# Optimization experiments

Hardware: AMD Instinct MI355X
Metric: run time of the kernel (lower is better)

Reference implementation:

```python
import jax, jax.numpy as jnp
import numpy as np
from jax import lax

# Static config (matches init_kwargs)
DIM = 256; DR = 4; GROUP = 2; NH = 4; KS = 3; NA = 1; NUM_CLASS = 80; MUL = 5.0
CR = DIM // DR            # reduced dim = 64
GC = CR // GROUP          # offset-group channels = 32
HC = CR // NH             # per-head dim = 16
SCALE = HC ** -0.5
B, H, W = 8, 64, 64


def setup_inputs() -> dict:
    key = jax.random.key(0)
    ks_ = jax.random.split(key, 8)
    x = jax.random.normal(ks_[0], (B, DIM, H, W), jnp.float32)
    # offset = absolute pixel coordinates of the base sampling grid
    offset = jax.random.uniform(ks_[1], (B, NA * 2 * KS * KS, H, W), jnp.float32) * (H - 1)
    return dict(
        x=x, offset=offset,
        ln1_g=jnp.ones((DIM,), jnp.float32), ln1_b=jnp.zeros((DIM,), jnp.float32),
        w_qkv=jax.random.normal(ks_[2], (3 * CR, DIM), jnp.float32) * 0.02,
        w_dw=jax.random.normal(ks_[3], (GC, 1, 3, 3), jnp.float32) * 0.1,
        ln2_g=jnp.ones((GC,), jnp.float32), ln2_b=jnp.zeros((GC,), jnp.float32),
        w_off=jax.random.normal(ks_[4], (NA * 2 * KS * KS, GC, 3, 3), jnp.float32) * 0.02,
        b_off=jnp.zeros((NA * 2 * KS * KS,), jnp.float32),
        rpb_table=jax.random.normal(ks_[5], (1, NH, 1, 1, KS * KS, HC), jnp.float32) * 0.02,
        w_proj=jax.random.normal(ks_[6], (DIM, CR), jnp.float32) * 0.02,
        b_proj=jnp.zeros((DIM,), jnp.float32),
        w_cls=jax.random.normal(ks_[7], (NUM_CLASS, DIM), jnp.float32) * 0.02,
        b_cls=jnp.zeros((NUM_CLASS,), jnp.float32),
    )


def _ln_chw(x, g, b, eps=1e-5):
    # LayerNorm over channel dim of NCHW tensor (LayerNormProxy)
    xt = jnp.moveaxis(x, 1, -1)
    m = xt.mean(-1, keepdims=True)
    v = ((xt - m) ** 2).mean(-1, keepdims=True)
    y = (xt - m) * lax.rsqrt(v + eps) * g + b
    return jnp.moveaxis(y, -1, 1)


def _conv(x, w, groups=1, pad=1):
    return lax.conv_general_dilated(x, w, (1, 1), [(pad, pad), (pad, pad)],
                                    feature_group_count=groups,
                                    dimension_numbers=('NCHW', 'OIHW', 'NCHW'))


def _grid_sample(img, grid):
    # img [N,C,H,W]; grid [N,Ho,Wo,2] with (x,y) in [-1,1]; bilinear, zeros pad, align_corners=True
    N, C, Hi, Wi = img.shape
    gx = (grid[..., 0] + 1.0) * 0.5 * (Wi - 1)
    gy = (grid[..., 1] + 1.0) * 0.5 * (Hi - 1)
    x0 = jnp.floor(gx); y0 = jnp.floor(gy)
    x1 = x0 + 1.0;      y1 = y0 + 1.0

    def gather(ix, iy):
        valid = (ix >= 0) & (ix <= Wi - 1) & (iy >= 0) & (iy <= Hi - 1)
        ixc = jnp.clip(ix, 0, Wi - 1).astype(jnp.int32)
        iyc = jnp.clip(iy, 0, Hi - 1).astype(jnp.int32)
        v = jax.vmap(lambda im, yy, xx: im[:, yy, xx])(img, iyc, ixc)  # [N,C,Ho,Wo]
        return v * valid[:, None].astype(img.dtype)

    wa = ((x1 - gx) * (y1 - gy))[:, None]
    wb = ((gx - x0) * (y1 - gy))[:, None]
    wc = ((x1 - gx) * (gy - y0))[:, None]
    wd = ((gx - x0) * (gy - y0))[:, None]
    return (gather(x0, y0) * wa + gather(x1, y0) * wb +
            gather(x0, y1) * wc + gather(x1, y1) * wd)


def _extract_feats(feat, off, Hh, Ww):
    # feat [Bg,GC,H,W]; off [Bg, NA*2*KS*KS, H, W] in pixel coords (row, col)
    Bg = feat.shape[0]
    o = off.reshape(Bg, NA, KS, KS, 2, Hh, Ww)
    o = o.transpose(0, 1, 2, 5, 3, 6, 4)                  # b na kh h kw w d
    o = o.reshape(Bg, NA * KS * Hh, KS * Ww, 2)
    gy = 2.0 * o[..., 0] / (Hh - 1) - 1.0                  # row coord
    gx = 2.0 * o[..., 1] / (Ww - 1) - 1.0                  # col coord
    grid = jnp.stack([gx, gy], -1)                         # flip(-1): (x, y)
    out = _grid_sample(feat, grid)                         # [Bg,GC,NA*KS*H,KS*W]
    out = out.reshape(Bg, GC, NA, KS, Hh, KS, Ww)
    out = out.transpose(0, 2, 3, 5, 1, 4, 6).reshape(Bg, NA * KS * KS, GC, Hh, Ww)
    return out


def reference(x, offset, ln1_g, ln1_b, w_qkv, w_dw, ln2_g, ln2_b, w_off, b_off,
              rpb_table, w_proj, b_proj, w_cls, b_cls):
    Bb, C, Hh, Ww = x.shape
    N = KS * KS

    x_ = _ln_chw(x, ln1_g, ln1_b)
    qkv = jnp.einsum('oc,bchw->bohw', w_qkv, x_)           # [B,3*CR,H,W]
    q, k, v = jnp.split(qkv, 3, axis=1)                    # each [B,CR,H,W]

    # --- offset prediction ---
    q_off = q.reshape(Bb * GROUP, GC, Hh, Ww)
    t = _conv(q_off, w_dw, groups=GC)                      # depthwise 3x3
    t = _ln_chw(t, ln2_g, ln2_b)
    t = jax.nn.gelu(t, approximate=False)
    pred_offset = _conv(t, w_off) + b_off[None, :, None, None]

    off = jnp.broadcast_to(offset[:, None], (Bb, GROUP, NA * 2 * N, Hh, Ww))
    off = off.reshape(Bb * GROUP, NA * 2 * N, Hh, Ww)
    off = jnp.tanh(pred_offset) * MUL + off

    # --- deformable gather of k/v ---
    k = _extract_feats(k.reshape(Bb * GROUP, GC, Hh, Ww), off, Hh, Ww)
    v = _extract_feats(v.reshape(Bb * GROUP, GC, Hh, Ww), off, Hh, Ww)

    def to_heads(t):
        # [(b g), na*n, gc, h, w] -> [b, nh, hw, na, n, hc]
        t = t.reshape(Bb, GROUP, NA, N, GC, Hh, Ww)
        t = t.transpose(0, 5, 6, 2, 3, 1, 4)               # b h w na n g gc
        t = t.reshape(Bb, Hh * Ww, NA, N, NH, HC)
        return t.transpose(0, 4, 1, 2, 3, 5)

    k = to_heads(k) + rpb_table                            # [B,NH,HW,NA,N,HC]
    v = to_heads(v)

    q = q.reshape(Bb, NH, HC, Hh * Ww).transpose(0, 1, 3, 2)  # [B,NH,HW,HC]
    q = jnp.broadcast_to((q * SCALE)[:, :, :, None, :], (Bb, NH, Hh * Ww, NA, HC))

    attn = jnp.einsum('bnpac,bnpakc->bnpak', q, k)         # [B,NH,HW,NA,N]
    attn = jax.nn.softmax(attn, axis=-1)
    out = jnp.einsum('bnpak,bnpakc->bnpac', attn, v)       # [B,NH,HW,NA,HC]

    out = out.transpose(0, 2, 3, 1, 4).reshape(Bb, Hh * Ww, NA, CR)
    out = out @ w_proj.T + b_proj                          # [B,HW,NA,C]
    out = out + x.transpose(0, 2, 3, 1).reshape(Bb, Hh * Ww, 1, C)

    cls = out @ w_cls.T + b_cls                            # [B,HW,NA,NUM_CLASS]
    cls = cls.reshape(Bb, Hh, Ww, NA, NUM_CLASS).transpose(0, 3, 4, 1, 2)
    return cls.reshape(Bb, NA * NUM_CLASS, Hh, Ww)
```

## Files before the change

kernel.cpp:

```cpp
#include <hip/hip_runtime.h>
#include <hip/hip_fp16.h>
#include <math.h>

#define BB   8
#define HW   4096
#define BHW  32768
#define DIM  256
#define CR   64
#define GC   32
#define NHD  4
#define HC   16
#define NTAP 9
#define NCLS 80

#define OFF_QP   0u
#define OFF_QT   2097152u
#define OFF_KT   4194304u
#define OFF_WBF  8388608u
#define OFF_AB   8437760u
#define OFF_T16  8650752u
#define OFF_OFFB 10485760u
#define OFF_WPT  13762560u
#define OFF_WCT  13778944u
#define OFF_WFT  13799424u

typedef short    bf16x8 __attribute__((ext_vector_type(8)));
typedef _Float16 f16x8  __attribute__((ext_vector_type(8)));
typedef float    f32x4  __attribute__((ext_vector_type(4)));

__device__ __forceinline__ unsigned short f2bf(float f) {
    unsigned u = __float_as_uint(f);
    unsigned r = u + 0x7FFFu + ((u >> 16) & 1u);
    return (unsigned short)(r >> 16);
}

__global__ __launch_bounds__(256) void k0_prep(
    const float* __restrict__ wqkv, const float* __restrict__ g1,
    const float* __restrict__ b1, const float* __restrict__ woff,
    const float* __restrict__ wproj, const float* __restrict__ wcls,
    float* __restrict__ ws)
{
    const int t = threadIdx.x;
    const int blk = blockIdx.x;
    if (blk < 192) {
        const int o = blk;
        unsigned short* wbf = (unsigned short*)(ws + OFF_WBF);
        wbf[o * 256 + t] = f2bf(wqkv[o * 256 + t] * g1[t]);
    } else if (blk < 448) {
        const int r = blk - 192;
        unsigned short* wpb = (unsigned short*)(ws + OFF_WPT);
        unsigned short* wcb = (unsigned short*)(ws + OFF_WCT);
        if (t < 64) wpb[r * 64 + t] = f2bf(wproj[r * 64 + t]);
        if (r < 80) wcb[r * 256 + t] = f2bf(wcls[r * 256 + t]);
    } else if (blk < 640) {
        const int o = blk - 448;
        __shared__ float sa[4], sb[4];
        float w = wqkv[o * 256 + t];
        float a = w * g1[t];
        float bb = w * b1[t];
        #pragma unroll
        for (int off = 1; off < 64; off <<= 1) {
            a  += __shfl_xor(a,  off, 64);
            bb += __shfl_xor(bb, off, 64);
        }
        const int wv = t >> 6;
        if ((t & 63) == 0) { sa[wv] = a; sb[wv] = bb; }
        __syncthreads();
        if (t == 0) {
            ws[OFF_AB + o]       = sa[0] + sa[1] + sa[2] + sa[3];
            ws[OFF_AB + 192 + o] = sb[0] + sb[1] + sb[2] + sb[3];
        }
    } else {
        int idx = (blk - 640) * 256 + t;
        if (idx < 2 * 9 * 64 * 8) {
            int j = idx & 7;
            int lane = (idx >> 3) & 63;
            int mw = idx >> 9;
            int m = mw / 9, wo = mw % 9;
            int o = m * 16 + (lane & 15);
            int ic = (lane >> 4) * 8 + j;
            float v = (o < 18) ? woff[(o * 32 + ic) * 9 + wo] : 0.f;
            ((__half*)(ws + OFF_WFT))[idx] = __float2half(v);
        }
    }
}

__global__ __launch_bounds__(512) void k1_mfma(
    const float* __restrict__ x, float* __restrict__ ws)
{
    __shared__ float tile[64 * 193];
    const int t = threadIdx.x;
    const int b = blockIdx.x & 7, row = blockIdx.x >> 3;
    const int wv = __builtin_amdgcn_readfirstlane(t >> 6);
    const int pt = wv & 3, oh = wv >> 2;
    const int lane = t & 63;
    const int quad = lane >> 4, pxl = lane & 15;
    const int colbase = row * 64 + pt * 16 + pxl;
    const unsigned short* wbf = (const unsigned short*)(ws + OFF_WBF);
    const float* AB = ws + OFF_AB;

    f32x4 acc[6];
    #pragma unroll
    for (int ot = 0; ot < 6; ++ot) acc[ot] = (f32x4){0.f, 0.f, 0.f, 0.f};
    float s = 0.f, ss = 0.f;
    const size_t xb0 = (size_t)b * DIM * HW + colbase;

    for (int ks = 0; ks < 8; ++ks) {
        const int cbase = ks * 32 + quad * 8;
        float xv[8];
        #pragma unroll
        for (int j = 0; j < 8; ++j) {
            xv[j] = x[xb0 + (size_t)(cbase + j) * HW];
            s += xv[j]; ss += xv[j] * xv[j];
        }
        union { bf16x8 v; unsigned short u[8]; } bfrag;
        #pragma unroll
        for (int j = 0; j < 8; ++j) bfrag.u[j] = f2bf(xv[j]);
        #pragma unroll
        for (int ot = 0; ot < 6; ++ot) {
            const int orow = (oh * 6 + ot) * 16 + pxl;
            union { float4 f; bf16x8 v; } afrag;
            afrag.f = *(const float4*)&wbf[orow * 256 + cbase];
            acc[ot] = __builtin_amdgcn_mfma_f32_16x16x32_bf16(afrag.v, bfrag.v, acc[ot], 0, 0, 0);
        }
    }

    s  += __shfl_xor(s, 16, 64);  s  += __shfl_xor(s, 32, 64);
    ss += __shfl_xor(ss, 16, 64); ss += __shfl_xor(ss, 32, 64);
    const float m = s * (1.f / 256.f);
    const float rsv = rsqrtf(ss * (1.f / 256.f) - m * m + 1e-5f);

    const int px = pt * 16 + pxl;
    #pragma unroll
    for (int ot = 0; ot < 6; ++ot) {
        #pragma unroll
        for (int r = 0; r < 4; ++r) {
            int o = (oh * 6 + ot) * 16 + quad * 4 + r;
            tile[px * 193 + o] = rsv * (acc[ot][r] - m * AB[o]) + AB[192 + o];
        }
    }
    __syncthreads();

    float*  qp  = ws + OFF_QP;
    __half* qth = (__half*)(ws + OFF_QT);
    __half* kvh = (__half*)(ws + OFF_KT);
    const int colrow = row * 64;
    #pragma unroll
    for (int it = 0; it < 8; ++it) {
        int idx = it * 512 + t;
        int o = idx >> 6, px2 = idx & 63;
        qp[(size_t)(b * 64 + o) * HW + colrow + px2] = tile[px2 * 193 + o];
    }
    #pragma unroll
    for (int it = 0; it < 8; ++it) {
        int idx = it * 512 + t;
        int px2 = idx >> 6, o = idx & 63;
        qth[(size_t)(b * HW + colrow + px2) * 64 + o] = __float2half(tile[px2 * 193 + o]);
    }
    #pragma unroll
    for (int it = 0; it < 4; ++it) {
        int idx = it * 512 + t;
        int px2 = idx >> 5, ch32 = idx & 31;
        int sB = ch32 >> 4, ch = ch32 & 15;
        kvh[(size_t)((2 * b) * HW + colrow + px2) * 64 + sB * 32 + ch]
            = __float2half(tile[px2 * 193 + 64 + ch32]);
    }
    #pragma unroll
    for (int it = 0; it < 4; ++it) {
        int idx = it * 512 + t;
        int px2 = idx >> 5, ch32 = idx & 31;
        int sB = ch32 >> 4, ch = ch32 & 15;
        kvh[(size_t)((2 * b + 1) * HW + colrow + px2) * 64 + sB * 32 + ch]
            = __float2half(tile[px2 * 193 + 96 + ch32]);
    }
    #pragma unroll
    for (int it = 0; it < 4; ++it) {
        int idx = it * 512 + t;
        int px2 = idx >> 5, ch32 = idx & 31;
        int sB = ch32 >> 4, ch = ch32 & 15;
        kvh[(size_t)((2 * b) * HW + colrow + px2) * 64 + sB * 32 + 16 + ch]
            = __float2half(tile[px2 * 193 + 128 + ch32]);
    }
    #pragma unroll
    for (int it = 0; it < 4; ++it) {
        int idx = it * 512 + t;
        int px2 = idx >> 5, ch32 = idx & 31;
        int sB = ch32 >> 4, ch = ch32 & 15;
        kvh[(size_t)((2 * b + 1) * HW + colrow + px2) * 64 + sB * 32 + 16 + ch]
            = __float2half(tile[px2 * 193 + 160 + ch32]);
    }
}

__global__ __launch_bounds__(256) void k2_off_feat(
    const float* __restrict__ wdw, const float* __restrict__ g2, const float* __restrict__ b2,
    float* __restrict__ ws)
{
    __shared__ float qtile[3][32][64];
    __shared__ float rsum[4][64], rsq[4][64], smv[64], srv[64];
    const int t = threadIdx.x;
    const int b = blockIdx.x & 7;
    const int rest = blockIdx.x >> 3;
    const int g = rest & 1;
    const int row = rest >> 1;
    const int bg = b * 2 + g;
    const int p = t & 63;
    const int cq = __builtin_amdgcn_readfirstlane(t >> 6);
    const float* qp = ws + OFF_QP;

    #pragma unroll
    for (int it = 0; it < 6; ++it) {
        int idx = it * 256 + t;
        int rc = idx >> 4;
        int seg = (idx & 15) << 2;
        int dyy = rc >> 5, ch = rc & 31;
        int y = row + dyy - 1;
        float4 v = make_float4(0.f, 0.f, 0.f, 0.f);
        if ((unsigned)y < 64u)
            v = *(const float4*)&qp[(size_t)(b * 64 + g * 32 + ch) * HW + y * 64 + seg];
        *(float4*)&qtile[dyy][ch][seg] = v;
    }
    __syncthreads();

    float vals[8];
    float s = 0.f, ss = 0.f;
    #pragma unroll
    for (int i = 0; i < 8; ++i) {
        int ch = cq * 8 + i;
        float a = 0.f;
        #pragma unroll
        for (int dy = 0; dy < 3; ++dy) {
            #pragma unroll
            for (int dx = 0; dx < 3; ++dx) {
                int xx = p + dx - 1;
                bool vld = (unsigned)xx < 64u;
                float q = qtile[dy][ch][vld ? xx : 0];
                a += (vld ? q : 0.f) * wdw[ch * 9 + dy * 3 + dx];
            }
        }
        vals[i] = a; s += a; ss += a * a;
    }
    rsum[cq][p] = s; rsq[cq][p] = ss;
    __syncthreads();
    if (t < 64) {
        float S = rsum[0][t] + rsum[1][t] + rsum[2][t] + rsum[3][t];
        float Q = rsq[0][t] + rsq[1][t] + rsq[2][t] + rsq[3][t];
        float m = S * (1.f / 32.f);
        float v = Q * (1.f / 32.f) - m * m;
        smv[t] = m; srv[t] = rsqrtf(v + 1e-5f);
    }
    __syncthreads();
    float m = smv[p], rv = srv[p];
    __half* tb16 = (__half*)(ws + OFF_T16);
    #pragma unroll
    for (int i = 0; i < 8; ++i) {
        int ch = cq * 8 + i;
        float u = (vals[i] - m) * rv * g2[ch] + b2[ch];
        vals[i] = 0.5f * u * (1.f + erff(u * 0.70710678118654752f));
    }
    union { float4 f; __half2 h[4]; } o16;
    #pragma unroll
    for (int i = 0; i < 4; ++i) o16.h[i] = __floats2half2_rn(vals[2 * i], vals[2 * i + 1]);
    *(float4*)&tb16[((size_t)bg * HW + row * 64 + p) * 32 + cq * 8] = o16.f;
}

__global__ __launch_bounds__(256) void k3_mfma(
    const float* __restrict__ boff, const float* __restrict__ off_in,
    float* __restrict__ ws)
{
    const int t = threadIdx.x;
    const int b = blockIdx.x & 7;
    const int rest = blockIdx.x >> 3;
    const int g = rest & 1;
    const int rowgrp = (rest >> 1) & 15;
    const int xh = rest >> 5;
    const int wv = __builtin_amdgcn_readfirstlane(t >> 6);
    const int lane = t & 63;
    const int quad = lane >> 4, pxl = lane & 15;
    const int row = rowgrp * 4 + wv;
    const int bg = b * 2 + g;
    const __half* t16 = (const __half*)(ws + OFF_T16);
    const __half* wfA = (const __half*)(ws + OFF_WFT);

    f32x4 acc[2][2];
    #pragma unroll
    for (int i = 0; i < 2; ++i)
        #pragma unroll
        for (int j = 0; j < 2; ++j) acc[i][j] = (f32x4){0.f, 0.f, 0.f, 0.f};

    union FH { float4 f; f16x8 h; };
    #pragma unroll
    for (int wo = 0; wo < 9; ++wo) {
        const int dy = wo / 3, dx = wo % 3;
        const int y = row + dy - 1;
        const bool yv = (unsigned)y < 64u;
        FH a0, a1;
        a0.f = *(const float4*)&wfA[(size_t)((0 * 9 + wo) * 64 + lane) * 8];
        a1.f = *(const float4*)&wfA[(size_t)((1 * 9 + wo) * 64 + lane) * 8];
        #pragma unroll
        for (int tile = 0; tile < 2; ++tile) {
            const int x = xh * 32 + tile * 16 + pxl + dx - 1;
            FH bf;
            bf.f = make_float4(0.f, 0.f, 0.f, 0.f);
            if (yv && (unsigned)x < 64u)
                bf.f = *(const float4*)&t16[((size_t)bg * HW + y * 64 + x) * 32 + quad * 8];
            acc[tile][0] = __builtin_amdgcn_mfma_f32_16x16x32_f16(a0.h, bf.h, acc[tile][0], 0, 0, 0);
            acc[tile][1] = __builtin_amdgcn_mfma_f32_16x16x32_f16(a1.h, bf.h, acc[tile][1], 0, 0, 0);
        }
    }

    float* ob = ws + OFF_OFFB;
    #pragma unroll
    for (int tile = 0; tile < 2; ++tile) {
        const int px = xh * 32 + tile * 16 + pxl;
        #pragma unroll
        for (int mi = 0; mi < 2; ++mi) {
            #pragma unroll
            for (int r = 0; r < 4; ++r) {
                int o = mi * 16 + quad * 4 + r;
                if (o < 18) {
                    float v = acc[tile][mi][r] + boff[o];
                    v = tanhf(v) * 5.0f + off_in[(size_t)(b * 18 + o) * HW + row * 64 + px];
                    ob[(size_t)(bg * 18 + o) * HW + row * 64 + px] = v;
                }
            }
        }
    }
}

__global__ __launch_bounds__(256, 4) void k45_attn_proj(
    const float* __restrict__ rpb, const float* __restrict__ x,
    const float* __restrict__ bproj, const float* __restrict__ bcls,
    float* __restrict__ ws, float* __restrict__ out)
{
    __shared__ float rpb_l[NHD * NTAP * HC];
    __shared__ unsigned short ao_l[16][72];
    __shared__ unsigned short tmp[16][264];
    for (int i = threadIdx.x; i < NHD * NTAP * HC; i += 256) rpb_l[i] = rpb[i];
    __syncthreads();

    const int t = threadIdx.x;
    const int wave = __builtin_amdgcn_readfirstlane(t >> 6);
    const int g = wave & 1, pxh = wave >> 1;
    const int lane = t & 63;
    const int pxl = lane & 7;
    const int prt = lane >> 3;
    const int s    = prt >> 2;
    const int half = (prt >> 1) & 1;
    const int j    = prt & 1;
    const int b = blockIdx.x & 7;
    const int chunk = blockIdx.x >> 3;
    const int hw_base = chunk * 16;
    const int hw = hw_base + pxh * 8 + pxl;
    const int pix = b * HW + hw;
    const int bg = b * 2 + g;
    const int head = g * 2 + s;

    const __half* qth = (const __half*)(ws + OFF_QT);
    const __half* kvh = (const __half*)(ws + OFF_KT);
    const float*  ob  = ws + OFF_OFFB;

    float rr_[NTAP], cc_[NTAP];
    #pragma unroll
    for (int n = 0; n < NTAP; ++n) {
        rr_[n] = ob[(size_t)(bg * 18 + 2 * n) * HW + hw];
        cc_[n] = ob[(size_t)(bg * 18 + 2 * n + 1) * HW + hw];
    }

    union F4H { float4 f; __half2 h[4]; };
    F4H qld;
    qld.f = *(const float4*)&qth[(size_t)pix * 64 + g * 32 + s * 16 + j * 8];
    const float qs = half ? 0.0f : 0.25f;
    float qv[8];
    #pragma unroll
    for (int i = 0; i < 4; ++i) {
        float2 q2 = __half22float2(qld.h[i]);
        qv[2 * i] = q2.x * qs; qv[2 * i + 1] = q2.y * qs;
    }

    const float4* rb4 = (const float4*)(rpb_l + head * (NTAP * HC) + j * 8);
    const __half* kvp = kvh + (size_t)(bg * HW) * 64 + prt * 8;

    __half2 av[NTAP][4];
    float logit[NTAP];

    #pragma unroll
    for (int n = 0; n < NTAP; ++n) {
        float r = rr_[n];
        float c = cc_[n];
        float y0f = floorf(r), x0f = floorf(c);
        float fy = r - y0f, fx = c - x0f;
        int iy0 = (int)y0f, ix0 = (int)x0f;
        float wts[4] = { (1.f - fx) * (1.f - fy), fx * (1.f - fy),
                         (1.f - fx) * fy,         fx * fy };
        __half2 acc0 = __float2half2_rn(0.f), acc1 = acc0, acc2 = acc0, acc3 = acc0;
        #pragma unroll
        for (int corner = 0; corner < 4; ++corner) {
            int cxx = ix0 + (corner & 1);
            int cyy = iy0 + (corner >> 1);
            bool vld = ((unsigned)cxx < 64u) && ((unsigned)cyy < 64u);
            float w = vld ? wts[corner] : 0.f;
            int cxc = min(max(cxx, 0), 63);
            int cyc = min(max(cyy, 0), 63);
            F4H kv;
            kv.f = *(const float4*)&kvp[(size_t)(cyc * 64 + cxc) * 64];
            __half2 w2 = __float2half2_rn(w);
            acc0 = __hfma2(kv.h[0], w2, acc0);
            acc1 = __hfma2(kv.h[1], w2, acc1);
            acc2 = __hfma2(kv.h[2], w2, acc2);
            acc3 = __hfma2(kv.h[3], w2, acc3);
        }
        av[n][0] = acc0; av[n][1] = acc1; av[n][2] = acc2; av[n][3] = acc3;
        float4 r0 = rb4[n * 4], r1 = rb4[n * 4 + 1];
        float2 a0 = __half22float2(acc0), a1 = __half22float2(acc1);
        float2 a2 = __half22float2(acc2), a3 = __half22float2(acc3);
        float part = qv[0] * (a0.x + r0.x) + qv[1] * (a0.y + r0.y)
                   + qv[2] * (a1.x + r0.z) + qv[3] * (a1.y + r0.w)
                   + qv[4] * (a2.x + r1.x) + qv[5] * (a2.y + r1.y)
                   + qv[6] * (a3.x + r1.z) + qv[7] * (a3.y + r1.w);
        part += __shfl_xor(part, 8, 64);
        part += __shfl_xor(part, 16, 64);
        logit[n] = part;
    }

    float m = logit[0];
    #pragma unroll
    for (int n = 1; n < NTAP; ++n) m = fmaxf(m, logit[n]);
    float l = 0.f;
    #pragma unroll
    for (int n = 0; n < NTAP; ++n) { logit[n] = __expf(logit[n] - m); l += logit[n]; }
    const float inv = 1.f / l;

    __half2 o0 = __float2half2_rn(0.f), o1 = o0, o2 = o0, o3 = o0;
    #pragma unroll
    for (int n = 0; n < NTAP; ++n) {
        __half2 p2 = __float2half2_rn(logit[n]);
        o0 = __hfma2(av[n][0], p2, o0);
        o1 = __hfma2(av[n][1], p2, o1);
        o2 = __hfma2(av[n][2], p2, o2);
        o3 = __hfma2(av[n][3], p2, o3);
    }
    if (half) {
        const int cb = head * 16 + j * 8;
        float2 f0 = __half22float2(o0), f1 = __half22float2(o1);
        float2 f2 = __half22float2(o2), f3 = __half22float2(o3);
        union { float4 f; unsigned short u[8]; } pk;
        pk.u[0] = f2bf(f0.x * inv); pk.u[1] = f2bf(f0.y * inv);
        pk.u[2] = f2bf(f1.x * inv); pk.u[3] = f2bf(f1.y * inv);
        pk.u[4] = f2bf(f2.x * inv); pk.u[5] = f2bf(f2.y * inv);
        pk.u[6] = f2bf(f3.x * inv); pk.u[7] = f2bf(f3.y * inv);
        *(float4*)&ao_l[pxh * 8 + pxl][cb] = pk.f;
    }
    __syncthreads();

    const int q4  = lane >> 4;
    const int p16 = lane & 15;
    const unsigned short* wpb = (const unsigned short*)(ws + OFF_WPT);
    const unsigned short* wcb = (const unsigned short*)(ws + OFF_WCT);

    union FB { float4 f; bf16x8 v; };
    FB bf0, bf1;
    bf0.f = *(const float4*)&ao_l[p16][q4 * 8];
    bf1.f = *(const float4*)&ao_l[p16][32 + q4 * 8];

    #pragma unroll
    for (int ot = wave * 4; ot < wave * 4 + 4; ++ot) {
        f32x4 acc = (f32x4){0.f, 0.f, 0.f, 0.f};
        FB a0, a1;
        const int om = ot * 16 + p16;
        a0.f = *(const float4*)&wpb[om * 64 + q4 * 8];
        a1.f = *(const float4*)&wpb[om * 64 + 32 + q4 * 8];
        acc = __builtin_amdgcn_mfma_f32_16x16x32_bf16(a0.v, bf0.v, acc, 0, 0, 0);
        acc = __builtin_amdgcn_mfma_f32_16x16x32_bf16(a1.v, bf1.v, acc, 0, 0, 0);
        union { unsigned short u[4]; } pk;
        #pragma unroll
        for (int r = 0; r < 4; ++r) {
            int o = ot * 16 + q4 * 4 + r;
            float v = acc[r] + bproj[o] + x[(size_t)(b * DIM + o) * HW + hw_base + p16];
            pk.u[r] = f2bf(v);
        }
        *(ushort4*)&tmp[p16][ot * 16 + q4 * 4] = *(ushort4*)pk.u;
    }
    __syncthreads();

    #pragma unroll
    for (int oc = wave; oc < 5; oc += 4) {
        f32x4 acc2 = (f32x4){0.f, 0.f, 0.f, 0.f};
        #pragma unroll
        for (int kc = 0; kc < 8; ++kc) {
            FB bb, aa;
            bb.f = *(const float4*)&tmp[p16][kc * 32 + q4 * 8];
            aa.f = *(const float4*)&wcb[(oc * 16 + p16) * 256 + kc * 32 + q4 * 8];
            acc2 = __builtin_amdgcn_mfma_f32_16x16x32_bf16(aa.v, bb.v, acc2, 0, 0, 0);
        }
        #pragma unroll
        for (int r = 0; r < 4; ++r) {
            int o = oc * 16 + q4 * 4 + r;
            out[(size_t)(b * NCLS + o) * HW + hw_base + p16] = acc2[r] + bcls[o];
        }
    }
}

extern "C" void kernel_launch(void* const* d_in, const int* in_sizes, int n_in,
                              void* d_out, int out_size, void* d_ws, size_t ws_size,
                              hipStream_t stream)
{
    const float* x     = (const float*)d_in[0];
    const float* off   = (const float*)d_in[1];
    const float* g1    = (const float*)d_in[2];
    const float* b1    = (const float*)d_in[3];
    const float* wqkv  = (const float*)d_in[4];
    const float* wdw   = (const float*)d_in[5];
    const float* g2    = (const float*)d_in[6];
    const float* b2    = (const float*)d_in[7];
    const float* woff  = (const float*)d_in[8];
    const float* boff  = (const float*)d_in[9];
    const float* rpb   = (const float*)d_in[10];
    const float* wproj = (const float*)d_in[11];
    const float* bproj = (const float*)d_in[12];
    const float* wcls  = (const float*)d_in[13];
    const float* bcls  = (const float*)d_in[14];
    float* ws  = (float*)d_ws;
    float* out = (float*)d_out;

    hipLaunchKernelGGL(k0_prep,       dim3(676),  dim3(256), 0, stream, wqkv, g1, b1, woff, wproj, wcls, ws);
    hipLaunchKernelGGL(k1_mfma,       dim3(512),  dim3(512), 0, stream, x, ws);
    hipLaunchKernelGGL(k2_off_feat,   dim3(1024), dim3(256), 0, stream, wdw, g2, b2, ws);
    hipLaunchKernelGGL(k3_mfma,       dim3(512),  dim3(256), 0, stream, boff, off, ws);
    hipLaunchKernelGGL(k45_attn_proj, dim3(2048), dim3(256), 0, stream, rpb, x, bproj, bcls, ws, out);
}
```

Measured before the change: 200.7 us.

## Fuse offset conv into attention kernel, keeping offsets in shared memory

Drops the separate offset-convolution kernel and computes the 3x3 offset conv via MFMA inside the attention kernel, one 16-pixel chunk per block. Each block splits the nine taps across wave pairs, reduces the partial sums through shared memory, applies tanh and the base offset, and stages the 18 offset channels in LDS. This removes one kernel launch and the global write and read of the offset buffer. In exchange it adds two block barriers, reuses the tmp LDS buffer, and gives each block smaller MFMA work with poorer reuse of the t16 halo loads.

```diff
diff --git a/kernel.cpp b/kernel.cpp
--- a/kernel.cpp
+++ b/kernel.cpp
@@ -263,80 +263,16 @@
     *(float4*)&tb16[((size_t)bg * HW + row * 64 + p) * 32 + cq * 8] = o16.f;
 }
 
-__global__ __launch_bounds__(256) void k3_mfma(
-    const float* __restrict__ boff, const float* __restrict__ off_in,
-    float* __restrict__ ws)
-{
-    const int t = threadIdx.x;
-    const int b = blockIdx.x & 7;
-    const int rest = blockIdx.x >> 3;
-    const int g = rest & 1;
-    const int rowgrp = (rest >> 1) & 15;
-    const int xh = rest >> 5;
-    const int wv = __builtin_amdgcn_readfirstlane(t >> 6);
-    const int lane = t & 63;
-    const int quad = lane >> 4, pxl = lane & 15;
-    const int row = rowgrp * 4 + wv;
-    const int bg = b * 2 + g;
-    const __half* t16 = (const __half*)(ws + OFF_T16);
-    const __half* wfA = (const __half*)(ws + OFF_WFT);
-
-    f32x4 acc[2][2];
-    #pragma unroll
-    for (int i = 0; i < 2; ++i)
-        #pragma unroll
-        for (int j = 0; j < 2; ++j) acc[i][j] = (f32x4){0.f, 0.f, 0.f, 0.f};
-
-    union FH { float4 f; f16x8 h; };
-    #pragma unroll
-    for (int wo = 0; wo < 9; ++wo) {
-        const int dy = wo / 3, dx = wo % 3;
-        const int y = row + dy - 1;
-        const bool yv = (unsigned)y < 64u;
-        FH a0, a1;
-        a0.f = *(const float4*)&wfA[(size_t)((0 * 9 + wo) * 64 + lane) * 8];
-        a1.f = *(const float4*)&wfA[(size_t)((1 * 9 + wo) * 64 + lane) * 8];
-        #pragma unroll
-        for (int tile = 0; tile < 2; ++tile) {
-            const int x = xh * 32 + tile * 16 + pxl + dx - 1;
-            FH bf;
-            bf.f = make_float4(0.f, 0.f, 0.f, 0.f);
-            if (yv && (unsigned)x < 64u)
-                bf.f = *(const float4*)&t16[((size_t)bg * HW + y * 64 + x) * 32 + quad * 8];
-            acc[tile][0] = __builtin_amdgcn_mfma_f32_16x16x32_f16(a0.h, bf.h, acc[tile][0], 0, 0, 0);
-            acc[tile][1] = __builtin_amdgcn_mfma_f32_16x16x32_f16(a1.h, bf.h, acc[tile][1], 0, 0, 0);
-        }
-    }
-
-    float* ob = ws + OFF_OFFB;
-    #pragma unroll
-    for (int tile = 0; tile < 2; ++tile) {
-        const int px = xh * 32 + tile * 16 + pxl;
-        #pragma unroll
-        for (int mi = 0; mi < 2; ++mi) {
-            #pragma unroll
-            for (int r = 0; r < 4; ++r) {
-                int o = mi * 16 + quad * 4 + r;
-                if (o < 18) {
-                    float v = acc[tile][mi][r] + boff[o];
-                    v = tanhf(v) * 5.0f + off_in[(size_t)(b * 18 + o) * HW + row * 64 + px];
-                    ob[(size_t)(bg * 18 + o) * HW + row * 64 + px] = v;
-                }
-            }
-        }
-    }
-}
-
 __global__ __launch_bounds__(256, 4) void k45_attn_proj(
     const float* __restrict__ rpb, const float* __restrict__ x,
     const float* __restrict__ bproj, const float* __restrict__ bcls,
+    const float* __restrict__ boff, const float* __restrict__ off_in,
     float* __restrict__ ws, float* __restrict__ out)
 {
     __shared__ float rpb_l[NHD * NTAP * HC];
     __shared__ unsigned short ao_l[16][72];
     __shared__ unsigned short tmp[16][264];
     for (int i = threadIdx.x; i < NHD * NTAP * HC; i += 256) rpb_l[i] = rpb[i];
-    __syncthreads();
 
     const int t = threadIdx.x;
     const int wave = __builtin_amdgcn_readfirstlane(t >> 6);
@@ -354,16 +290,77 @@
     const int pix = b * HW + hw;
     const int bg = b * 2 + g;
     const int head = g * 2 + s;
+    const int pxb = pxh * 8 + pxl;
+
+    {
+        const int bgc = wave & 1;
+        const int th  = wave >> 1;
+        const int q4c = lane >> 4;
+        const int pc  = lane & 15;
+        const int y0r = hw_base >> 6;
+        const int x0c = hw_base & 63;
+        const int bgg = b * 2 + bgc;
+        const __half* t16 = (const __half*)(ws + OFF_T16);
+        const __half* wfA = (const __half*)(ws + OFF_WFT);
+        f32x4* accL = (f32x4*)tmp;
+        float* obl  = (float*)tmp + 1024;
+
+        f32x4 ca0 = (f32x4){0.f, 0.f, 0.f, 0.f}, ca1 = ca0;
+        union FH { float4 f; f16x8 h; };
+        const int wo_beg = th * 5, wo_end = th ? 9 : 5;
+        for (int wo = wo_beg; wo < wo_end; ++wo) {
+            const int dy = wo / 3, dx = wo % 3;
+            const int yy = y0r + dy - 1;
+            const bool yv = (unsigned)yy < 64u;
+            const int xx = x0c + pc + dx - 1;
+            FH bf; bf.f = make_float4(0.f, 0.f, 0.f, 0.f);
+            if (yv && (unsigned)xx < 64u)
+                bf.f = *(const float4*)&t16[((size_t)bgg * HW + yy * 64 + xx) * 32 + q4c * 8];
+            FH a0, a1;
+            a0.f = *(const float4*)&wfA[(size_t)((0 * 9 + wo) * 64 + lane) * 8];
+            a1.f = *(const float4*)&wfA[(size_t)((1 * 9 + wo) * 64 + lane) * 8];
+            ca0 = __builtin_amdgcn_mfma_f32_16x16x32_f16(a0.h, bf.h, ca0, 0, 0, 0);
+            ca1 = __builtin_amdgcn_mfma_f32_16x16x32_f16(a1.h, bf.h, ca1, 0, 0, 0);
+        }
+        if (th == 1) {
+            accL[(bgc * 2 + 0) * 64 + lane] = ca0;
+            accL[(bgc * 2 + 1) * 64 + lane] = ca1;
+        }
+        __syncthreads();
+        if (th == 0) {
+            f32x4 s0 = accL[(bgc * 2 + 0) * 64 + lane];
+            f32x4 s1 = accL[(bgc * 2 + 1) * 64 + lane];
+            #pragma unroll
+            for (int r = 0; r < 4; ++r) { ca0[r] += s0[r]; ca1[r] += s1[r]; }
+            #pragma unroll
+            for (int r = 0; r < 4; ++r) {
+                int o = q4c * 4 + r;
+                float v = ca0[r] + boff[o];
+                v = tanhf(v) * 5.0f + off_in[(size_t)(b * 18 + o) * HW + hw_base + pc];
+                obl[(bgc * 18 + o) * 16 + pc] = v;
+            }
+            if (q4c == 0) {
+                #pragma unroll
+                for (int r = 0; r < 2; ++r) {
+                    int o = 16 + r;
+                    float v = ca1[r] + boff[o];
+                    v = tanhf(v) * 5.0f + off_in[(size_t)(b * 18 + o) * HW + hw_base + pc];
+                    obl[(bgc * 18 + o) * 16 + pc] = v;
+                }
+            }
+        }
+        __syncthreads();
+    }
 
     const __half* qth = (const __half*)(ws + OFF_QT);
     const __half* kvh = (const __half*)(ws + OFF_KT);
-    const float*  ob  = ws + OFF_OFFB;
+    const float*  obl = (const float*)tmp + 1024;
 
     float rr_[NTAP], cc_[NTAP];
     #pragma unroll
     for (int n = 0; n < NTAP; ++n) {
-        rr_[n] = ob[(size_t)(bg * 18 + 2 * n) * HW + hw];
-        cc_[n] = ob[(size_t)(bg * 18 + 2 * n + 1) * HW + hw];
+        rr_[n] = obl[(g * 18 + 2 * n) * 16 + pxb];
+        cc_[n] = obl[(g * 18 + 2 * n + 1) * 16 + pxb];
     }
 
     union F4H { float4 f; __half2 h[4]; };
@@ -448,7 +445,7 @@
         pk.u[2] = f2bf(f1.x * inv); pk.u[3] = f2bf(f1.y * inv);
         pk.u[4] = f2bf(f2.x * inv); pk.u[5] = f2bf(f2.y * inv);
         pk.u[6] = f2bf(f3.x * inv); pk.u[7] = f2bf(f3.y * inv);
-        *(float4*)&ao_l[pxh * 8 + pxl][cb] = pk.f;
+        *(float4*)&ao_l[pxb][cb] = pk.f;
     }
     __syncthreads();
 
@@ -525,6 +522,5 @@
     hipLaunchKernelGGL(k0_prep,       dim3(676),  dim3(256), 0, stream, wqkv, g1, b1, woff, wproj, wcls, ws);
     hipLaunchKernelGGL(k1_mfma,       dim3(512),  dim3(512), 0, stream, x, ws);
     hipLaunchKernelGGL(k2_off_feat,   dim3(1024), dim3(256), 0, stream, wdw, g2, b2, ws);
-    hipLaunchKernelGGL(k3_mfma,       dim3(512),  dim3(256), 0, stream, boff, off, ws);
-    hipLaunchKernelGGL(k45_attn_proj, dim3(2048), dim3(256), 0, stream, rpb, x, bproj, bcls, ws, out);
+    hipLaunchKernelGGL(k45_attn_proj, dim3(2048), dim3(256), 0, stream, rpb, x, bproj, bcls, boff, off, ws, out);
 }
```

New measurement: 203.3 us. No clear change (+1.3%).
